# Performance work log

Hardware: AMD Instinct MI355X
Metric: run time of the kernel (lower is better)

## Reference

```python
import jax, jax.numpy as jnp
import numpy as np

N = 150000        # active voxels
C = 64            # channels
G = 64            # n_groups (depthwise)
CI = C // G       # in channels per group = 1
CO = C // G       # out channels per group = 1
K = 27            # 3x3x3 kernel volume
BS = 2            # batch size
SS = (480, 360, 32)  # spatial shape (z, y, x)


def _build_pairs(rng):
    """Build submanifold conv indice pairs (gather/scatter maps) from real voxel geometry."""
    total = SS[0] * SS[1] * SS[2]
    per_b = N // BS
    idx_list = []
    for b in range(BS):
        flat = rng.choice(total, size=per_b, replace=False)
        z = flat // (SS[1] * SS[2])
        rem = flat % (SS[1] * SS[2])
        y = rem // SS[2]
        x = rem % SS[2]
        idx_list.append(np.stack([np.full(per_b, b), z, y, x], 1))
    indices = np.concatenate(idx_list).astype(np.int64)  # [N, 4] (b,z,y,x)
    mult = np.array([total, SS[1] * SS[2], SS[2], 1], dtype=np.int64)
    keys = indices @ mult
    order = np.argsort(keys)
    sk = keys[order]
    offsets = np.array([(dz, dy, dx) for dz in (-1, 0, 1) for dy in (-1, 0, 1) for dx in (-1, 0, 1)], dtype=np.int64)
    pair_in = np.zeros((K, N), np.int64)
    pair_out = np.zeros((K, N), np.int64)
    mask = np.zeros((K, N), np.bool_)
    ar = np.arange(N, dtype=np.int64)
    for k in range(K):
        nb = indices.copy()
        nb[:, 1:] += offsets[k]
        inb = ((nb[:, 1] >= 0) & (nb[:, 1] < SS[0]) &
               (nb[:, 2] >= 0) & (nb[:, 2] < SS[1]) &
               (nb[:, 3] >= 0) & (nb[:, 3] < SS[2]))
        nk = nb @ mult
        pos = np.clip(np.searchsorted(sk, nk), 0, N - 1)
        found = inb & (sk[pos] == nk)
        j = order[pos]
        pair_in[k] = np.where(found, j, 0)
        pair_out[k] = np.where(found, ar, 0)
        mask[k] = found
    return pair_in, pair_out, mask


def setup_inputs() -> dict:
    rng = np.random.default_rng(0)
    pair_in, pair_out, pair_mask = _build_pairs(rng)
    key = jax.random.key(0)
    kf, kw, kb = jax.random.split(key, 3)
    features = jax.random.normal(kf, (N, C), dtype=jnp.float32)
    weight = jax.random.normal(kw, (K, G, CI, CO), dtype=jnp.float32) * 0.1
    bias = jax.random.normal(kb, (G * CO,), dtype=jnp.float32)
    return {"features": features, "weight": weight, "bias": bias,
            "pair_in": jnp.asarray(pair_in), "pair_out": jnp.asarray(pair_out),
            "pair_mask": jnp.asarray(pair_mask)}


def reference(features, weight, bias, pair_in, pair_out, pair_mask):
    # Grouped submanifold sparse conv: gather -> grouped matmul -> scatter-add,
    # scanned over the K kernel offsets to keep peak memory at O(N*C).
    n = features.shape[0]
    f = features.reshape(n, G, CI)
    mask_f = pair_mask.astype(features.dtype)

    def body(out, kd):
        pin, pout, m, w = kd  # pin/pout: [N], m: [N], w: [G, CI, CO]
        g = f[pin] * m[:, None, None]                 # [N, G, CI] masked gather
        contrib = jnp.einsum('ngc,gco->ngo', g, w)    # grouped matmul
        return out.at[pout].add(contrib), None

    out0 = jnp.zeros((n, G, CO), features.dtype)
    out, _ = jax.lax.scan(body, out0, (pair_in, pair_out, mask_f, weight))
    return out.reshape(n, G * CO) + bias
```

## Files before the change

### kernel.cpp

```cpp
#include <hip/hip_runtime.h>


#define KVOL 27
#define VPW  4
#define WPB  4

__global__ __launch_bounds__(256) void spconv_meta_kernel(
    const int* __restrict__ pair_in,
    const int* __restrict__ pair_mask,
    unsigned int* __restrict__ bits_ws,
    int n)
{
    const int vox = blockIdx.x * 256 + threadIdx.x;
    if (vox >= n) return;

    unsigned int bits = 0;
    #pragma unroll
    for (int k = 0; k < KVOL; ++k) {
        const int mv = pair_mask[(size_t)k * n + vox];
        bits |= (mv != 0 ? 1u : 0u) << k;
    }
    const int pin13 = pair_in[(size_t)13 * n + vox];
    if ((bits & (1u << 13)) && pin13 == vox)
        bits = (bits & ~(1u << 13)) | 0x80000000u;

    bits_ws[vox] = bits;
}

__global__ __launch_bounds__(256) void spconv_dw_kernel(
    const float* __restrict__ features,
    const float* __restrict__ weight,
    const float* __restrict__ bias,
    const int* __restrict__ pair_in,
    const unsigned int* __restrict__ bits_ws,
    float* __restrict__ out,
    int n)
{
    const int t     = threadIdx.x;
    const int w     = t >> 6;
    const int c     = t & 63;
    const int vbase = blockIdx.x * (VPW * WPB) + w * VPW;

    unsigned int bitsv[VPW];
    float fc[VPW];
    #pragma unroll
    for (int s = 0; s < VPW; ++s) { bitsv[s] = 0; fc[s] = 0.0f; }

    #pragma unroll
    for (int s = 0; s < VPW; ++s) {
        const int vox = vbase + s;
        if (vox < n) {
            bitsv[s] = bits_ws[vox];
            fc[s]    = features[(size_t)vox * 64 + c];
        }
    }

    const float b   = bias[c];
    const float w13 = weight[13 * 64 + c];

    #pragma unroll
    for (int s = 0; s < VPW; ++s) {
        const int vox = vbase + s;
        if (vox >= n) break;

        const unsigned int bv = __builtin_amdgcn_readfirstlane(bitsv[s]);
        float acc = b;

        if (bv & 0x80000000u)
            acc = fmaf(fc[s], w13, acc);

        unsigned int found = bv & 0x07FFFFFFu;
        while (found) {
            const int k = __builtin_ctz(found);
            found &= found - 1;
            const int pin = pair_in[(size_t)k * n + vox];
            acc = fmaf(features[(size_t)pin * 64 + c], weight[k * 64 + c], acc);
        }

        __builtin_nontemporal_store(acc, &out[(size_t)vox * 64 + c]);
    }
}

extern "C" void kernel_launch(void* const* d_in, const int* in_sizes, int n_in,
                              void* d_out, int out_size, void* d_ws, size_t ws_size,
                              hipStream_t stream) {
    const float* features  = (const float*)d_in[0];
    const float* weight    = (const float*)d_in[1];
    const float* bias      = (const float*)d_in[2];
    const int* pair_in     = (const int*)d_in[3];
    const int* pair_mask   = (const int*)d_in[5];
    float* out             = (float*)d_out;
    unsigned int* bits_ws  = (unsigned int*)d_ws;

    const int n = in_sizes[0] / 64;

    const int blocks1 = (n + 255) / 256;
    spconv_meta_kernel<<<blocks1, 256, 0, stream>>>(pair_in, pair_mask, bits_ws, n);

    const int vpb = VPW * WPB;
    const int blocks2 = (n + vpb - 1) / vpb;
    spconv_dw_kernel<<<blocks2, 256, 0, stream>>>(
        features, weight, bias, pair_in, bits_ws, out, n);
}
```

Before: 133.7 us.

## Vectorize depthwise conv with float4 lanes, four voxels per wavefront

Each wavefront now handles four voxels at a time, with 16 lanes per voxel loading float4 channel chunks, in place of one voxel per wavefront with one float per lane. The per-voxel neighbor masks are OR-ed across the four voxels with shuffles into one uniform loop, and a 0/1 select discards neighbors a voxel does not have. This is meant to cut scalar loop overhead and issue wider gather loads. In exchange, each voxel's loop runs over the union of all four masks, so it does extra masked loads, and the four voxels' gathers are no longer contiguous.

New measurement: 132.3 us. About the same (-1.1%).

```diff
diff --git a/kernel.cpp b/kernel.cpp
--- a/kernel.cpp
+++ b/kernel.cpp
@@ -2,8 +2,8 @@
 
 
 #define KVOL 27
-#define VPW  4
-#define WPB  4
+
+typedef float vf4 __attribute__((ext_vector_type(4)));
 
 __global__ __launch_bounds__(256) void spconv_meta_kernel(
     const int* __restrict__ pair_in,
@@ -27,6 +27,9 @@
     bits_ws[vox] = bits;
 }
 
+#define GPW  2
+#define VPB  32
+
 __global__ __launch_bounds__(256) void spconv_dw_kernel(
     const float* __restrict__ features,
     const float* __restrict__ weight,
@@ -38,46 +41,50 @@
 {
     const int t     = threadIdx.x;
     const int w     = t >> 6;
-    const int c     = t & 63;
-    const int vbase = blockIdx.x * (VPW * WPB) + w * VPW;
+    const int lane  = t & 63;
+    const int sub   = lane >> 4;
+    const int c4    = lane & 15;
+    const int wbase = blockIdx.x * VPB + w * (GPW * 4);
 
-    unsigned int bitsv[VPW];
-    float fc[VPW];
+    int voxl[GPW], voxc[GPW];
+    unsigned int bitsv[GPW];
+    vf4 fc[GPW];
     #pragma unroll
-    for (int s = 0; s < VPW; ++s) { bitsv[s] = 0; fc[s] = 0.0f; }
+    for (int g = 0; g < GPW; ++g) {
+        voxl[g] = wbase + g * 4 + sub;
+        voxc[g] = voxl[g] < n ? voxl[g] : (n - 1);
+        bitsv[g] = bits_ws[voxc[g]];
+        fc[g] = ((const vf4*)&features[(size_t)voxc[g] * 64])[c4];
+    }
+
+    const vf4 bv  = ((const vf4*)bias)[c4];
+    const vf4 w13 = ((const vf4*)&weight[13 * 64])[c4];
 
     #pragma unroll
-    for (int s = 0; s < VPW; ++s) {
-        const int vox = vbase + s;
-        if (vox < n) {
-            bitsv[s] = bits_ws[vox];
-            fc[s]    = features[(size_t)vox * 64 + c];
-        }
-    }
+    for (int g = 0; g < GPW; ++g) {
+        const unsigned int bits = bitsv[g];
 
-    const float b   = bias[c];
-    const float w13 = weight[13 * 64 + c];
+        const float m13 = (bits & 0x80000000u) ? 1.0f : 0.0f;
+        vf4 acc = bv + (fc[g] * m13) * w13;
 
-    #pragma unroll
-    for (int s = 0; s < VPW; ++s) {
-        const int vox = vbase + s;
-        if (vox >= n) break;
+        unsigned int res = bits & 0x07FFFFFFu;
+        unsigned int uni = res | __shfl_xor(res, 16);
+        uni |= __shfl_xor(uni, 32);
+        uni = __builtin_amdgcn_readfirstlane(uni);
 
-        const unsigned int bv = __builtin_amdgcn_readfirstlane(bitsv[s]);
-        float acc = b;
-
-        if (bv & 0x80000000u)
-            acc = fmaf(fc[s], w13, acc);
-
-        unsigned int found = bv & 0x07FFFFFFu;
-        while (found) {
-            const int k = __builtin_ctz(found);
-            found &= found - 1;
-            const int pin = pair_in[(size_t)k * n + vox];
-            acc = fmaf(features[(size_t)pin * 64 + c], weight[k * 64 + c], acc);
+        while (uni) {
+            const int k = __builtin_ctz(uni);
+            uni &= uni - 1;
+            const float sel = (res >> k) & 1u ? 1.0f : 0.0f;
+            const int pin = pair_in[(size_t)k * n + voxc[g]];
+            const vf4 f  = ((const vf4*)&features[(size_t)pin * 64])[c4];
+            const vf4 wk = ((const vf4*)&weight[k * 64])[c4];
+            acc += (f * sel) * wk;
         }
 
-        __builtin_nontemporal_store(acc, &out[(size_t)vox * 64 + c]);
+        if (voxl[g] < n)
+            __builtin_nontemporal_store(acc,
+                (vf4*)&out[(size_t)voxl[g] * 64 + c4 * 4]);
     }
 }
 
@@ -97,8 +104,7 @@
     const int blocks1 = (n + 255) / 256;
     spconv_meta_kernel<<<blocks1, 256, 0, stream>>>(pair_in, pair_mask, bits_ws, n);
 
-    const int vpb = VPW * WPB;
-    const int blocks2 = (n + vpb - 1) / vpb;
+    const int blocks2 = (n + VPB - 1) / VPB;
     spconv_dw_kernel<<<blocks2, 256, 0, stream>>>(
         features, weight, bias, pair_in, bits_ws, out, n);
 }
```
